# Optimization experiments

Hardware: AMD Instinct MI355X
Metric: run time of the kernel (lower is better)

## Reference

```python
import jax, jax.numpy as jnp
import numpy as np

NUM_HEADS = 8
BN_EPS = 1e-5


def setup_inputs() -> dict:
    key = jax.random.key(0)
    ks = jax.random.split(key, 7)
    B, C, T, N = 16, 512, 128, 64
    x = jax.random.normal(ks[0], (B, C, T, N), dtype=jnp.float32)
    # 1x1 convs stored as [out, in] matrices
    w_qkv = jax.random.normal(ks[1], (3 * C, C), dtype=jnp.float32) * (1.0 / np.sqrt(C))
    b_qkv = jax.random.normal(ks[2], (3 * C,), dtype=jnp.float32) * 0.01
    w_proj = jax.random.normal(ks[3], (C, C), dtype=jnp.float32) * (1.0 / np.sqrt(C))
    b_proj = jax.random.normal(ks[4], (C,), dtype=jnp.float32) * 0.01
    gamma = jnp.ones((C,), dtype=jnp.float32) + 0.1 * jax.random.normal(ks[5], (C,), dtype=jnp.float32)
    beta = 0.1 * jax.random.normal(ks[6], (C,), dtype=jnp.float32)
    return {"x": x, "w_qkv": w_qkv, "b_qkv": b_qkv, "w_proj": w_proj,
            "b_proj": b_proj, "gamma": gamma, "beta": beta}


def reference(x, w_qkv, b_qkv, w_proj, b_proj, gamma, beta):
    B, C, T, N = x.shape
    H = NUM_HEADS
    hd = C // H
    scale = 1.0 / np.sqrt(hd).astype(np.float32)

    # qkv 1x1 conv: [B,3C,T,N]
    qkv = jnp.einsum('bctn,oc->botn', x, w_qkv) + b_qkv[None, :, None, None]
    q, k, v = jnp.split(qkv, 3, axis=1)

    def to_heads(t):  # [B,C,T,N] -> [B,H,T,N,hd]
        return t.reshape(B, H, hd, T, N).transpose(0, 1, 3, 4, 2)

    q, k, v = to_heads(q), to_heads(k), to_heads(v)

    # unnormalized attention over the N (node) axis, no softmax
    attn = jnp.einsum('bhtnd,bhtmd->bhtnm', q, k) * scale  # [B,H,T,N,N]
    out = jnp.einsum('bhtnm,bhtmd->bhtnd', attn, v)        # [B,H,T,N,hd]

    # back to [B,C,T,N]
    out = out.transpose(0, 1, 4, 2, 3).reshape(B, C, T, N)

    # proj 1x1 conv
    out = jnp.einsum('bctn,oc->botn', out, w_proj) + b_proj[None, :, None, None]

    # BatchNorm2d (training-mode batch statistics, biased variance, eps=1e-5)
    mean = out.mean(axis=(0, 2, 3))
    var = out.var(axis=(0, 2, 3))
    out = (out - mean[None, :, None, None]) * (gamma / jnp.sqrt(var + BN_EPS))[None, :, None, None] \
          + beta[None, :, None, None]

    return out + x
```

## Files before the change

kernel.cpp:

```cpp
#include <hip/hip_runtime.h>

typedef unsigned int uint;
typedef unsigned short ushort;
typedef short short8 __attribute__((ext_vector_type(8)));
typedef float floatx4 __attribute__((ext_vector_type(4)));
typedef ushort ushortx8 __attribute__((ext_vector_type(8)));
typedef ushort ushortx4 __attribute__((ext_vector_type(4)));
typedef uint uintx4 __attribute__((ext_vector_type(4)));

#define DEV static __device__ __forceinline__

#define Bsz 16
#define Cch 512
#define Tt 128
#define Nn 64
#define Hh 8
#define HD 64
#define Pp 8192
#define BPOS 131072
#define C3 1536

DEV int swz(int row, int c8) { return row * 8 + (c8 ^ (row & 7) ^ ((row >> 3) & 7)); }

DEV ushort f2bf(float f) {
  uint u = __float_as_uint(f);
  return (ushort)((u + 0x7FFFu + ((u >> 16) & 1u)) >> 16);
}
DEV float bf2f(ushort h) { return __uint_as_float(((uint)h) << 16); }

DEV void gll16(const ushort* src, ushort* dst) {
  __builtin_amdgcn_global_load_lds(
      (const __attribute__((address_space(1))) unsigned int*)src,
      (__attribute__((address_space(3))) unsigned int*)dst, 16, 0, 0);
}

__global__ __launch_bounds__(256) void k_cvt(const float* __restrict__ src,
                                             ushort* __restrict__ dst, int n) {
  int gid = blockIdx.x * 256 + threadIdx.x;
  int i8 = gid * 8;
  if (i8 < n) {
    floatx4 a = *(const floatx4*)&src[i8];
    floatx4 b = *(const floatx4*)&src[i8 + 4];
    ushortx8 o;
#pragma unroll
    for (int j = 0; j < 4; ++j) { o[j] = f2bf(a[j]); o[j + 4] = f2bf(b[j]); }
    *(ushortx8*)&dst[i8] = o;
  }
}

__global__ __launch_bounds__(256) void k_transpose_x(const float* __restrict__ x,
                                                     ushort* __restrict__ xT) {
  int p0 = blockIdx.x * 64, c0 = blockIdx.y * 64, b = blockIdx.z;
  __shared__ __align__(16) ushort sm[4096];
  int tid = threadIdx.x;
  const float* xb = x + (size_t)b * Cch * Pp;
  ushort* xTb = xT + (size_t)b * Pp * Cch;
#pragma unroll
  for (int it = 0; it < 4; ++it) {
    int cc = tid + it * 256;
    int r = cc >> 4, c4 = cc & 15;
    floatx4 v = *(const floatx4*)&xb[(size_t)(c0 + r) * Pp + p0 + c4 * 4];
    ushortx4 o;
#pragma unroll
    for (int j = 0; j < 4; ++j) o[j] = f2bf(v[j]);
    *(ushortx4*)&sm[swz(r, c4 >> 1) * 8 + (c4 & 1) * 4] = o;
  }
  __syncthreads();
#pragma unroll
  for (int it = 0; it < 2; ++it) {
    int cc = tid + it * 256;
    int pl = cc >> 3, c8 = cc & 7;
    ushortx8 o;
#pragma unroll
    for (int j = 0; j < 8; ++j) {
      int c = c8 * 8 + j;
      o[j] = sm[swz(c, pl >> 3) * 8 + (pl & 7)];
    }
    *(ushortx8*)&xTb[(size_t)(p0 + pl) * Cch + c0 + c8 * 8] = o;
  }
}

__global__ __launch_bounds__(256) void k_gemm_bt(const ushort* __restrict__ A,
                                                 const ushort* __restrict__ W,
                                                 const float* __restrict__ bias,
                                                 ushort* __restrict__ D,
                                                 int K, int ldD,
                                                 size_t sAb, size_t sDb) {
  __shared__ __align__(16) ushort sm[32768];
  int tid = threadIdx.x;
  int lane = tid & 63, w = tid >> 6;
  int wm = (w & 1) * 64, wn = (w >> 1) * 64;
  size_t m0 = (size_t)blockIdx.y * 128;
  size_t n0 = (size_t)blockIdx.x * 128;
  const ushort* Ab = A + (size_t)blockIdx.z * sAb;
  ushort* Db = D + (size_t)blockIdx.z * sDb;

  const ushort *aS[4], *wS[4];
#pragma unroll
  for (int it = 0; it < 4; ++it) {
    int i = it * 256 + tid;
    int r = i >> 3;
    int c8 = (i & 7) ^ (r & 7) ^ ((r >> 3) & 7);
    aS[it] = &Ab[(m0 + r) * (size_t)K + c8 * 8];
    wS[it] = &W[(n0 + r) * (size_t)K + c8 * 8];
  }
  int dof = w * 512;

  floatx4 zero4 = {0.f, 0.f, 0.f, 0.f};
  floatx4 acc[4][4];
#pragma unroll
  for (int i = 0; i < 4; ++i)
#pragma unroll
    for (int j = 0; j < 4; ++j) acc[i][j] = zero4;

  const int NT = K >> 6;
#pragma unroll
  for (int it = 0; it < 4; ++it) {
    gll16(aS[it], &sm[it * 2048 + dof]);
    gll16(wS[it], &sm[8192 + it * 2048 + dof]);
  }
  __syncthreads();

  int cur = 0;
  for (int t = 0; t < NT; ++t) {
    ushort* cA = sm + (cur << 14);
    ushort* cB = cA + 8192;
    if (t + 1 < NT) {
      ushort* nA = sm + ((cur ^ 1) << 14);
      ushort* nB = nA + 8192;
      int kb = (t + 1) << 6;
#pragma unroll
      for (int it = 0; it < 4; ++it) {
        gll16(aS[it] + kb, &nA[it * 2048 + dof]);
        gll16(wS[it] + kb, &nB[it * 2048 + dof]);
      }
    }
#pragma unroll
    for (int kk = 0; kk < 2; ++kk) {
      int g = kk * 4 + (lane >> 4);
      int rr = lane & 15;
      short8 af[4], bf[4];
#pragma unroll
      for (int i = 0; i < 4; ++i) af[i] = *(const short8*)&cA[swz(wm + i * 16 + rr, g) * 8];
#pragma unroll
      for (int j = 0; j < 4; ++j) bf[j] = *(const short8*)&cB[swz(wn + j * 16 + rr, g) * 8];
#pragma unroll
      for (int i = 0; i < 4; ++i)
#pragma unroll
        for (int j = 0; j < 4; ++j)
          acc[i][j] = __builtin_amdgcn_mfma_f32_16x16x32_bf16(af[i], bf[j], acc[i][j], 0, 0, 0);
    }
    __syncthreads();
    cur ^= 1;
  }

  int quad = lane >> 4, col = lane & 15;
#pragma unroll
  for (int j = 0; j < 4; ++j) {
    int n_loc = wn + j * 16 + col;
    float bj = bias[n0 + n_loc];
#pragma unroll
    for (int i = 0; i < 4; ++i)
#pragma unroll
      for (int r = 0; r < 4; ++r) {
        int m_loc = wm + i * 16 + quad * 4 + r;
        sm[(m_loc * 16 + ((n_loc >> 3) ^ (m_loc & 7) ^ ((m_loc >> 3) & 7))) * 8 + (n_loc & 7)] =
            f2bf(acc[i][j][r] + bj);
      }
  }
  __syncthreads();
#pragma unroll
  for (int it = 0; it < 8; ++it) {
    int cc = tid + it * 256;
    int m_loc = cc >> 4, cn = cc & 15;
    uintx4 v = *(const uintx4*)&sm[(m_loc * 16 + (cn ^ (m_loc & 7) ^ ((m_loc >> 3) & 7))) * 8];
    *(uintx4*)&Db[(m0 + m_loc) * (size_t)ldD + n0 + cn * 8] = v;
  }
}

__global__ __launch_bounds__(256) void k_gemm2_t(const ushort* __restrict__ A,
                                                 const ushort* __restrict__ W,
                                                 const float* __restrict__ bias,
                                                 ushort* __restrict__ yL,
                                                 ushort* __restrict__ y0,
                                                 int K, int ldD,
                                                 size_t sAb, size_t sDb,
                                                 float* __restrict__ psum,
                                                 float* __restrict__ psq) {
  __shared__ __align__(16) ushort sm[32768];
  float* smf = (float*)sm;
  int tid = threadIdx.x;
  int lane = tid & 63, w = tid >> 6;
  int wm = (w & 1) * 64, wn = (w >> 1) * 64;
  size_t m0 = (size_t)blockIdx.y * 128;
  size_t n0 = (size_t)blockIdx.x * 128;
  const ushort* Ab = A + (size_t)blockIdx.z * sAb;
  ushort* Db = (blockIdx.z == 0) ? y0 : yL + (size_t)blockIdx.z * sDb;
  int part = blockIdx.z * 64 + blockIdx.y;

  const ushort *aS[4], *wS[4];
#pragma unroll
  for (int it = 0; it < 4; ++it) {
    int i = it * 256 + tid;
    int r = i >> 3;
    int c8 = (i & 7) ^ (r & 7) ^ ((r >> 3) & 7);
    aS[it] = &Ab[(m0 + r) * (size_t)K + c8 * 8];
    wS[it] = &W[(n0 + r) * (size_t)K + c8 * 8];
  }
  int dof = w * 512;

  floatx4 zero4 = {0.f, 0.f, 0.f, 0.f};
  floatx4 acc[4][4];
#pragma unroll
  for (int i = 0; i < 4; ++i)
#pragma unroll
    for (int j = 0; j < 4; ++j) acc[i][j] = zero4;

  const int NT = K >> 6;
#pragma unroll
  for (int it = 0; it < 4; ++it) {
    gll16(aS[it], &sm[it * 2048 + dof]);
    gll16(wS[it], &sm[8192 + it * 2048 + dof]);
  }
  __syncthreads();

  int cur = 0;
  for (int t = 0; t < NT; ++t) {
    ushort* cA = sm + (cur << 14);
    ushort* cB = cA + 8192;
    if (t + 1 < NT) {
      ushort* nA = sm + ((cur ^ 1) << 14);
      ushort* nB = nA + 8192;
      int kb = (t + 1) << 6;
#pragma unroll
      for (int it = 0; it < 4; ++it) {
        gll16(aS[it] + kb, &nA[it * 2048 + dof]);
        gll16(wS[it] + kb, &nB[it * 2048 + dof]);
      }
    }
#pragma unroll
    for (int kk = 0; kk < 2; ++kk) {
      int g = kk * 4 + (lane >> 4);
      int rr = lane & 15;
      short8 af[4], bf[4];
#pragma unroll
      for (int i = 0; i < 4; ++i) af[i] = *(const short8*)&cA[swz(wm + i * 16 + rr, g) * 8];
#pragma unroll
      for (int j = 0; j < 4; ++j) bf[j] = *(const short8*)&cB[swz(wn + j * 16 + rr, g) * 8];
#pragma unroll
      for (int i = 0; i < 4; ++i)
#pragma unroll
        for (int j = 0; j < 4; ++j)
          acc[i][j] = __builtin_amdgcn_mfma_f32_16x16x32_bf16(af[i], bf[j], acc[i][j], 0, 0, 0);
    }
    __syncthreads();
    cur ^= 1;
  }

  int quad = lane >> 4, col = lane & 15;
#pragma unroll
  for (int h = 0; h < 2; ++h) {
    __syncthreads();
    if ((w >> 1) == h) {
#pragma unroll
      for (int j = 0; j < 4; ++j) {
        int n1 = j * 16 + col;
        float bj = bias[n0 + h * 64 + n1];
#pragma unroll
        for (int i = 0; i < 4; ++i) {
          int mb = wm + i * 16 + quad * 4;
          floatx4 v4;
#pragma unroll
          for (int r = 0; r < 4; ++r) v4[r] = acc[i][j][r] + bj;
          *(floatx4*)&smf[n1 * 128 + (mb ^ ((n1 & 7) << 2))] = v4;
        }
      }
    }
    __syncthreads();
#pragma unroll
    for (int it = 0; it < 8; ++it) {
      int cc = tid + it * 256;
      int n2 = cc >> 5, ck = cc & 31;
      floatx4 v = *(const floatx4*)&smf[n2 * 128 + ((ck * 4) ^ ((n2 & 7) << 2))];
      ushortx4 o;
#pragma unroll
      for (int r = 0; r < 4; ++r) o[r] = f2bf(v[r]);
      *(ushortx4*)&Db[(n0 + h * 64 + n2) * (size_t)ldD + m0 + ck * 4] = o;
      float s = 0.f, q = 0.f;
#pragma unroll
      for (int r = 0; r < 4; ++r) {
        float f = bf2f(o[r]);
        s += f;
        q += f * f;
      }
#pragma unroll
      for (int off = 16; off > 0; off >>= 1) {
        s += __shfl_down(s, off, 32);
        q += __shfl_down(q, off, 32);
      }
      if ((tid & 31) == 0) {
        size_t c = n0 + h * 64 + n2;
        psum[c * 1024 + part] = s;
        psq[c * 1024 + part] = q;
      }
    }
  }
}

__global__ __launch_bounds__(256) void k_attn(const ushort* __restrict__ qkv,
                                              ushort* __restrict__ aT,
                                              size_t sQb, size_t sAb) {
  int bx = blockIdx.x;
  int t = bx & 127, h = bx >> 7;
  __shared__ __align__(16) ushort sm[16384];
  ushort* qs = sm;
  ushort* ks = sm + 4096;
  ushort* vt = sm + 8192;
  ushort* ss = sm + 12288;
  int tid = threadIdx.x, lane = tid & 63, w = tid >> 6;
  int quad = lane >> 4, col = lane & 15;
  const ushort* base = qkv + (size_t)blockIdx.y * sQb + (size_t)(t * 64) * C3 + h * 64;

#pragma unroll
  for (int it = 0; it < 2; ++it) {
    int i = it * 256 + tid;
    int r = i >> 3;
    int c8 = (i & 7) ^ (r & 7) ^ ((r >> 3) & 7);
    gll16(&base[(size_t)r * C3 + c8 * 8], &qs[(size_t)(it * 256 + w * 64) * 8]);
    gll16(&base[(size_t)r * C3 + 512 + c8 * 8], &ks[(size_t)(it * 256 + w * 64) * 8]);
    int n = i >> 3, d8 = i & 7;
    ushortx8 vv = *(const ushortx8*)&base[(size_t)n * C3 + 1024 + d8 * 8];
#pragma unroll
    for (int j = 0; j < 8; ++j) {
      int dp = d8 * 8 + j;
      vt[swz(dp, n >> 3) * 8 + (n & 7)] = vv[j];
    }
  }
  __syncthreads();

  floatx4 zero4 = {0.f, 0.f, 0.f, 0.f};
  floatx4 accs[4] = {zero4, zero4, zero4, zero4};
#pragma unroll
  for (int kk = 0; kk < 2; ++kk) {
    int g = kk * 4 + quad;
    short8 aq = *(const short8*)&qs[swz(w * 16 + col, g) * 8];
#pragma unroll
    for (int j = 0; j < 4; ++j) {
      short8 bk = *(const short8*)&ks[swz(j * 16 + col, g) * 8];
      accs[j] = __builtin_amdgcn_mfma_f32_16x16x32_bf16(aq, bk, accs[j], 0, 0, 0);
    }
  }
#pragma unroll
  for (int j = 0; j < 4; ++j)
#pragma unroll
    for (int r = 0; r < 4; ++r) {
      int n = w * 16 + quad * 4 + r, m = j * 16 + col;
      ss[swz(n, m >> 3) * 8 + (m & 7)] = f2bf(accs[j][r] * 0.125f);
    }
  __syncthreads();

  floatx4 acco[4] = {zero4, zero4, zero4, zero4};
#pragma unroll
  for (int kk = 0; kk < 2; ++kk) {
    int g = kk * 4 + quad;
    short8 as = *(const short8*)&ss[swz(w * 16 + col, g) * 8];
#pragma unroll
    for (int j = 0; j < 4; ++j) {
      short8 bv = *(const short8*)&vt[swz(j * 16 + col, g) * 8];
      acco[j] = __builtin_amdgcn_mfma_f32_16x16x32_bf16(as, bv, acco[j], 0, 0, 0);
    }
  }
#pragma unroll
  for (int j = 0; j < 4; ++j)
#pragma unroll
    for (int r = 0; r < 4; ++r) {
      int n = w * 16 + quad * 4 + r, dp = j * 16 + col;
      qs[swz(n, dp >> 3) * 8 + (dp & 7)] = f2bf(acco[j][r]);
    }
  __syncthreads();
  ushort* aTb = aT + (size_t)blockIdx.y * sAb + (size_t)(t * 64) * Cch + h * 64;
#pragma unroll
  for (int it = 0; it < 2; ++it) {
    int cc = tid + it * 256;
    int n = cc >> 3, c8 = cc & 7;
    uintx4 v = *(const uintx4*)&qs[swz(n, c8) * 8];
    *(uintx4*)&aTb[(size_t)n * Cch + c8 * 8] = v;
  }
}

__global__ __launch_bounds__(256) void k_bnfin(const float* __restrict__ psum,
                                               const float* __restrict__ psq,
                                               const float* __restrict__ gamma,
                                               const float* __restrict__ beta,
                                               float* __restrict__ scaleS,
                                               float* __restrict__ shiftS) {
  int c = blockIdx.x;
  int tid = threadIdx.x;
  floatx4 v = *(const floatx4*)&psum[(size_t)c * 1024 + tid * 4];
  floatx4 u = *(const floatx4*)&psq[(size_t)c * 1024 + tid * 4];
  float s = v[0] + v[1] + v[2] + v[3];
  float q = u[0] + u[1] + u[2] + u[3];
#pragma unroll
  for (int off = 32; off > 0; off >>= 1) {
    s += __shfl_down(s, off);
    q += __shfl_down(q, off);
  }
  __shared__ float rs[4], rq[4];
  if ((tid & 63) == 0) { rs[tid >> 6] = s; rq[tid >> 6] = q; }
  __syncthreads();
  if (tid == 0) {
    float S = rs[0] + rs[1] + rs[2] + rs[3];
    float Q = rq[0] + rq[1] + rq[2] + rq[3];
    float inv = 1.0f / (float)BPOS;
    float mean = S * inv;
    float var = Q * inv - mean * mean;
    float sc = gamma[c] * rsqrtf(var + 1e-5f);
    scaleS[c] = sc;
    shiftS[c] = beta[c] - mean * sc;
  }
}

__global__ __launch_bounds__(256) void k_final(const float* __restrict__ x,
                                               const ushort* __restrict__ y,
                                               float* __restrict__ out,
                                               const float* __restrict__ scaleS,
                                               const float* __restrict__ shiftS) {
  size_t gid = (size_t)blockIdx.x * 256 + threadIdx.x;
  size_t i8 = gid * 8;
  int c = (int)((i8 >> 13) & 511);
  float sc = scaleS[c], sh = shiftS[c];
  ushortx8 yv = *(const ushortx8*)&y[i8];
  floatx4 x0 = *(const floatx4*)&x[i8];
  floatx4 x1 = *(const floatx4*)&x[i8 + 4];
  floatx4 o0, o1;
#pragma unroll
  for (int j = 0; j < 4; ++j) {
    o0[j] = bf2f(yv[j]) * sc + sh + x0[j];
    o1[j] = bf2f(yv[j + 4]) * sc + sh + x1[j];
  }
  *(floatx4*)&out[i8] = o0;
  *(floatx4*)&out[i8 + 4] = o1;
}

extern "C" void kernel_launch(void* const* d_in, const int* in_sizes, int n_in,
                              void* d_out, int out_size, void* d_ws, size_t ws_size,
                              hipStream_t stream) {
  const float* x      = (const float*)d_in[0];
  const float* w_qkv  = (const float*)d_in[1];
  const float* b_qkv  = (const float*)d_in[2];
  const float* w_proj = (const float*)d_in[3];
  const float* b_proj = (const float*)d_in[4];
  const float* gamma  = (const float*)d_in[5];
  const float* beta   = (const float*)d_in[6];
  float* outf = (float*)d_out;

  char* ws = (char*)d_ws;
  float*  psum   = (float*)ws;
  float*  psq    = (float*)(ws + 2097152ull);
  ushort* y0ws   = (ushort*)(ws + 4194304ull);
  ushort* wqkvb  = (ushort*)(ws + 33554432ull);
  ushort* wprojb = (ushort*)(ws + 35127296ull);
  float*  st     = (float*)(ws + 35651584ull);
  float* scaleS = st, *shiftS = st + 512;

  ushort* xT   = (ushort*)((char*)d_out + 134217728ull);
  ushort* qkvL = (ushort*)d_out;
  ushort* yL   = (ushort*)d_out;

  const size_t PC = (size_t)Pp * Cch;
  const size_t PQ = (size_t)Pp * C3;
  const size_t CP = (size_t)Cch * Pp;

  k_cvt<<<dim3(384), 256, 0, stream>>>(w_qkv, wqkvb, 3 * Cch * Cch);
  k_cvt<<<dim3(128), 256, 0, stream>>>(w_proj, wprojb, Cch * Cch);
  k_transpose_x<<<dim3(Pp / 64, Cch / 64, Bsz), 256, 0, stream>>>(x, xT);

  for (int g = 0; g < 3; ++g) {
    int b0 = g * 5;
    k_gemm_bt<<<dim3(C3 / 128, Pp / 128, 5), 256, 0, stream>>>(
        xT + (size_t)b0 * PC, wqkvb, b_qkv, qkvL, Cch, C3, PC, PQ);
    k_attn<<<dim3(Hh * Tt, 5), 256, 0, stream>>>(qkvL, xT + (size_t)b0 * PC, PQ, PC);
  }
  k_gemm_bt<<<dim3(C3 / 128, Pp / 128, 1), 256, 0, stream>>>(
      xT + 15 * PC, wqkvb, b_qkv, qkvL, Cch, C3, 0, 0);
  k_attn<<<dim3(Hh * Tt, 1), 256, 0, stream>>>(qkvL, xT + 15 * PC, 0, 0);

  k_gemm2_t<<<dim3(Cch / 128, Pp / 128, 16), 256, 0, stream>>>(
      xT, wprojb, b_proj, yL, y0ws, Cch, Pp, PC, PC, psum, psq);

  k_bnfin<<<dim3(Cch), 256, 0, stream>>>(psum, psq, gamma, beta, scaleS, shiftS);

  k_final<<<dim3(8 * 2048), 256, 0, stream>>>(x + 8 * CP, yL + 8 * PC, outf + 8 * CP, scaleS, shiftS);
  k_final<<<dim3(4 * 2048), 256, 0, stream>>>(x + 4 * CP, yL + 4 * PC, outf + 4 * CP, scaleS, shiftS);
  k_final<<<dim3(2 * 2048), 256, 0, stream>>>(x + 2 * CP, yL + 2 * PC, outf + 2 * CP, scaleS, shiftS);
  k_final<<<dim3(1 * 2048), 256, 0, stream>>>(x + 1 * CP, yL + 1 * PC, outf + 1 * CP, scaleS, shiftS);
  k_final<<<dim3(1 * 2048), 256, 0, stream>>>(x, y0ws, outf, scaleS, shiftS);
}
```

Baseline: 1.157 ms.

## Fuse QKV projection and per-node attention into one kernel per (batch, t)

Replaces the batched QKV GEMM plus separate attention kernels with one fused kernel. Each block loads a 64-position by 512-channel input tile into LDS, then loops over heads: it computes Q/K/V with MFMA, forms the scores, applies them to V, and writes the result back in place. This removes the large QKV intermediate round-trip through global memory and several launches. In exchange, weights are read straight from global/L2 by every block with no LDS staging, and the 112KB of dynamic LDS limits occupancy to one block per CU.

```diff
diff --git a/kernel.cpp b/kernel.cpp
--- a/kernel.cpp
+++ b/kernel.cpp
@@ -80,101 +80,181 @@
   }
 }
 
-__global__ __launch_bounds__(256) void k_gemm_bt(const ushort* __restrict__ A,
-                                                 const ushort* __restrict__ W,
-                                                 const float* __restrict__ bias,
-                                                 ushort* __restrict__ D,
-                                                 int K, int ldD,
-                                                 size_t sAb, size_t sDb) {
-  __shared__ __align__(16) ushort sm[32768];
-  int tid = threadIdx.x;
-  int lane = tid & 63, w = tid >> 6;
-  int wm = (w & 1) * 64, wn = (w >> 1) * 64;
-  size_t m0 = (size_t)blockIdx.y * 128;
-  size_t n0 = (size_t)blockIdx.x * 128;
-  const ushort* Ab = A + (size_t)blockIdx.z * sAb;
-  ushort* Db = D + (size_t)blockIdx.z * sDb;
-
-  const ushort *aS[4], *wS[4];
-#pragma unroll
-  for (int it = 0; it < 4; ++it) {
+__global__ __launch_bounds__(256) void k_qkv_attn(ushort* __restrict__ xaT,
+                                                  const ushort* __restrict__ Wk,
+                                                  const float* __restrict__ bq) {
+  extern __shared__ __align__(16) ushort sm[];
+  int tid = threadIdx.x, lane = tid & 63, w = tid >> 6;
+  int pair = w >> 1, wh = w & 1;
+  int quad = lane >> 4, col = lane & 15;
+  int rr = col;
+  int t = blockIdx.x, b = blockIdx.y;
+  ushort* xb = xaT + ((size_t)b * Pp + (size_t)t * 64) * Cch;
+
+#pragma unroll
+  for (int it = 0; it < 16; ++it) {
     int i = it * 256 + tid;
-    int r = i >> 3;
+    int kt = i >> 9, r = (i >> 3) & 63;
     int c8 = (i & 7) ^ (r & 7) ^ ((r >> 3) & 7);
-    aS[it] = &Ab[(m0 + r) * (size_t)K + c8 * 8];
-    wS[it] = &W[(n0 + r) * (size_t)K + c8 * 8];
-  }
-  int dof = w * 512;
-
+    gll16(&xb[(size_t)r * Cch + kt * 64 + c8 * 8], &sm[(it * 256 + w * 64) * 8]);
+  }
+  __syncthreads();
+
+  ushort* qs = sm + 32768 + pair * 12288;
+  ushort* ks = qs + 4096;
+  ushort* vt = qs + 8192;
   floatx4 zero4 = {0.f, 0.f, 0.f, 0.f};
-  floatx4 acc[4][4];
-#pragma unroll
-  for (int i = 0; i < 4; ++i)
-#pragma unroll
-    for (int j = 0; j < 4; ++j) acc[i][j] = zero4;
-
-  const int NT = K >> 6;
-#pragma unroll
-  for (int it = 0; it < 4; ++it) {
-    gll16(aS[it], &sm[it * 2048 + dof]);
-    gll16(wS[it], &sm[8192 + it * 2048 + dof]);
-  }
-  __syncthreads();
-
-  int cur = 0;
-  for (int t = 0; t < NT; ++t) {
-    ushort* cA = sm + (cur << 14);
-    ushort* cB = cA + 8192;
-    if (t + 1 < NT) {
-      ushort* nA = sm + ((cur ^ 1) << 14);
-      ushort* nB = nA + 8192;
-      int kb = (t + 1) << 6;
-#pragma unroll
-      for (int it = 0; it < 4; ++it) {
-        gll16(aS[it] + kb, &nA[it * 2048 + dof]);
-        gll16(wS[it] + kb, &nB[it * 2048 + dof]);
-      }
-    }
+
+  for (int hh = 0; hh < 4; ++hh) {
+    int h = pair * 4 + hh;
+    int rowQK = wh * 512 + h * 64;
+    int rowV = 1024 + h * 64 + wh * 32;
+
+    floatx4 acc[4][4];
+#pragma unroll
+    for (int i2 = 0; i2 < 4; ++i2)
+#pragma unroll
+      for (int j = 0; j < 4; ++j) acc[i2][j] = zero4;
+#pragma unroll
+    for (int kt = 0; kt < 8; ++kt)
+#pragma unroll
+      for (int kk = 0; kk < 2; ++kk) {
+        int g = kk * 4 + (lane >> 4);
+        const ushort* wb = &Wk[(size_t)(rowQK + rr) * Cch + kt * 64 + g * 8];
+        short8 af[4], bf[4];
+#pragma unroll
+        for (int i2 = 0; i2 < 4; ++i2)
+          af[i2] = *(const short8*)&sm[kt * 4096 + swz(i2 * 16 + rr, g) * 8];
+#pragma unroll
+        for (int j = 0; j < 4; ++j) bf[j] = *(const short8*)&wb[(size_t)(j * 16) * Cch];
+#pragma unroll
+        for (int i2 = 0; i2 < 4; ++i2)
+#pragma unroll
+          for (int j = 0; j < 4; ++j)
+            acc[i2][j] = __builtin_amdgcn_mfma_f32_16x16x32_bf16(af[i2], bf[j], acc[i2][j], 0, 0, 0);
+      }
+    {
+      ushort* dqk = wh ? ks : qs;
+#pragma unroll
+      for (int j = 0; j < 4; ++j) {
+        int d = j * 16 + col;
+        float bj = bq[rowQK + d];
+#pragma unroll
+        for (int i2 = 0; i2 < 4; ++i2)
+#pragma unroll
+          for (int r = 0; r < 4; ++r) {
+            int n = i2 * 16 + quad * 4 + r;
+            dqk[swz(n, d >> 3) * 8 + (d & 7)] = f2bf(acc[i2][j][r] + bj);
+          }
+      }
+    }
+
+    floatx4 accv[4][2];
+#pragma unroll
+    for (int i2 = 0; i2 < 4; ++i2)
+#pragma unroll
+      for (int j = 0; j < 2; ++j) accv[i2][j] = zero4;
+#pragma unroll
+    for (int kt = 0; kt < 8; ++kt)
+#pragma unroll
+      for (int kk = 0; kk < 2; ++kk) {
+        int g = kk * 4 + (lane >> 4);
+        const ushort* wb = &Wk[(size_t)(rowV + rr) * Cch + kt * 64 + g * 8];
+        short8 af[4], bf[2];
+#pragma unroll
+        for (int i2 = 0; i2 < 4; ++i2)
+          af[i2] = *(const short8*)&sm[kt * 4096 + swz(i2 * 16 + rr, g) * 8];
+#pragma unroll
+        for (int j = 0; j < 2; ++j) bf[j] = *(const short8*)&wb[(size_t)(j * 16) * Cch];
+#pragma unroll
+        for (int i2 = 0; i2 < 4; ++i2)
+#pragma unroll
+          for (int j = 0; j < 2; ++j)
+            accv[i2][j] = __builtin_amdgcn_mfma_f32_16x16x32_bf16(af[i2], bf[j], accv[i2][j], 0, 0, 0);
+      }
+#pragma unroll
+    for (int j = 0; j < 2; ++j) {
+      int d = wh * 32 + j * 16 + col;
+      float bj = bq[1024 + h * 64 + d];
+#pragma unroll
+      for (int i2 = 0; i2 < 4; ++i2)
+#pragma unroll
+        for (int r = 0; r < 4; ++r) {
+          int n = i2 * 16 + quad * 4 + r;
+          vt[swz(d, n >> 3) * 8 + (n & 7)] = f2bf(accv[i2][j][r] + bj);
+        }
+    }
+    __syncthreads();
+
+    floatx4 accs[4][2];
+#pragma unroll
+    for (int i2 = 0; i2 < 4; ++i2)
+#pragma unroll
+      for (int j = 0; j < 2; ++j) accs[i2][j] = zero4;
 #pragma unroll
     for (int kk = 0; kk < 2; ++kk) {
       int g = kk * 4 + (lane >> 4);
-      int rr = lane & 15;
-      short8 af[4], bf[4];
-#pragma unroll
-      for (int i = 0; i < 4; ++i) af[i] = *(const short8*)&cA[swz(wm + i * 16 + rr, g) * 8];
-#pragma unroll
-      for (int j = 0; j < 4; ++j) bf[j] = *(const short8*)&cB[swz(wn + j * 16 + rr, g) * 8];
-#pragma unroll
-      for (int i = 0; i < 4; ++i)
-#pragma unroll
-        for (int j = 0; j < 4; ++j)
-          acc[i][j] = __builtin_amdgcn_mfma_f32_16x16x32_bf16(af[i], bf[j], acc[i][j], 0, 0, 0);
-    }
-    __syncthreads();
-    cur ^= 1;
-  }
-
-  int quad = lane >> 4, col = lane & 15;
-#pragma unroll
-  for (int j = 0; j < 4; ++j) {
-    int n_loc = wn + j * 16 + col;
-    float bj = bias[n0 + n_loc];
-#pragma unroll
-    for (int i = 0; i < 4; ++i)
-#pragma unroll
-      for (int r = 0; r < 4; ++r) {
-        int m_loc = wm + i * 16 + quad * 4 + r;
-        sm[(m_loc * 16 + ((n_loc >> 3) ^ (m_loc & 7) ^ ((m_loc >> 3) & 7))) * 8 + (n_loc & 7)] =
-            f2bf(acc[i][j][r] + bj);
-      }
-  }
-  __syncthreads();
-#pragma unroll
-  for (int it = 0; it < 8; ++it) {
-    int cc = tid + it * 256;
-    int m_loc = cc >> 4, cn = cc & 15;
-    uintx4 v = *(const uintx4*)&sm[(m_loc * 16 + (cn ^ (m_loc & 7) ^ ((m_loc >> 3) & 7))) * 8];
-    *(uintx4*)&Db[(m0 + m_loc) * (size_t)ldD + n0 + cn * 8] = v;
+      short8 aq[4], bk[2];
+#pragma unroll
+      for (int i2 = 0; i2 < 4; ++i2) aq[i2] = *(const short8*)&qs[swz(i2 * 16 + rr, g) * 8];
+#pragma unroll
+      for (int j = 0; j < 2; ++j) bk[j] = *(const short8*)&ks[swz(wh * 32 + j * 16 + rr, g) * 8];
+#pragma unroll
+      for (int i2 = 0; i2 < 4; ++i2)
+#pragma unroll
+        for (int j = 0; j < 2; ++j)
+          accs[i2][j] = __builtin_amdgcn_mfma_f32_16x16x32_bf16(aq[i2], bk[j], accs[i2][j], 0, 0, 0);
+    }
+    __syncthreads();
+#pragma unroll
+    for (int j = 0; j < 2; ++j)
+#pragma unroll
+      for (int i2 = 0; i2 < 4; ++i2)
+#pragma unroll
+        for (int r = 0; r < 4; ++r) {
+          int n = i2 * 16 + quad * 4 + r, m = wh * 32 + j * 16 + col;
+          qs[swz(n, m >> 3) * 8 + (m & 7)] = f2bf(accs[i2][j][r] * 0.125f);
+        }
+    __syncthreads();
+
+    floatx4 acco[4][2];
+#pragma unroll
+    for (int i2 = 0; i2 < 4; ++i2)
+#pragma unroll
+      for (int j = 0; j < 2; ++j) acco[i2][j] = zero4;
+#pragma unroll
+    for (int kk = 0; kk < 2; ++kk) {
+      int g = kk * 4 + (lane >> 4);
+      short8 as[4], bv[2];
+#pragma unroll
+      for (int i2 = 0; i2 < 4; ++i2) as[i2] = *(const short8*)&qs[swz(i2 * 16 + rr, g) * 8];
+#pragma unroll
+      for (int j = 0; j < 2; ++j) bv[j] = *(const short8*)&vt[swz(wh * 32 + j * 16 + rr, g) * 8];
+#pragma unroll
+      for (int i2 = 0; i2 < 4; ++i2)
+#pragma unroll
+        for (int j = 0; j < 2; ++j)
+          acco[i2][j] = __builtin_amdgcn_mfma_f32_16x16x32_bf16(as[i2], bv[j], acco[i2][j], 0, 0, 0);
+    }
+#pragma unroll
+    for (int j = 0; j < 2; ++j)
+#pragma unroll
+      for (int i2 = 0; i2 < 4; ++i2)
+#pragma unroll
+        for (int r = 0; r < 4; ++r) {
+          int n = i2 * 16 + quad * 4 + r, d = wh * 32 + j * 16 + col;
+          ks[swz(n, d >> 3) * 8 + (d & 7)] = f2bf(acco[i2][j][r]);
+        }
+    __syncthreads();
+
+#pragma unroll
+    for (int it = 0; it < 4; ++it) {
+      int cc = it * 128 + wh * 64 + lane;
+      int n = cc >> 3, c8 = cc & 7;
+      uintx4 v = *(const uintx4*)&ks[swz(n, c8) * 8];
+      *(uintx4*)&xb[(size_t)n * Cch + h * 64 + c8 * 8] = v;
+    }
+    __syncthreads();
   }
 }
 
@@ -307,87 +387,6 @@
   }
 }
 
-__global__ __launch_bounds__(256) void k_attn(const ushort* __restrict__ qkv,
-                                              ushort* __restrict__ aT,
-                                              size_t sQb, size_t sAb) {
-  int bx = blockIdx.x;
-  int t = bx & 127, h = bx >> 7;
-  __shared__ __align__(16) ushort sm[16384];
-  ushort* qs = sm;
-  ushort* ks = sm + 4096;
-  ushort* vt = sm + 8192;
-  ushort* ss = sm + 12288;
-  int tid = threadIdx.x, lane = tid & 63, w = tid >> 6;
-  int quad = lane >> 4, col = lane & 15;
-  const ushort* base = qkv + (size_t)blockIdx.y * sQb + (size_t)(t * 64) * C3 + h * 64;
-
-#pragma unroll
-  for (int it = 0; it < 2; ++it) {
-    int i = it * 256 + tid;
-    int r = i >> 3;
-    int c8 = (i & 7) ^ (r & 7) ^ ((r >> 3) & 7);
-    gll16(&base[(size_t)r * C3 + c8 * 8], &qs[(size_t)(it * 256 + w * 64) * 8]);
-    gll16(&base[(size_t)r * C3 + 512 + c8 * 8], &ks[(size_t)(it * 256 + w * 64) * 8]);
-    int n = i >> 3, d8 = i & 7;
-    ushortx8 vv = *(const ushortx8*)&base[(size_t)n * C3 + 1024 + d8 * 8];
-#pragma unroll
-    for (int j = 0; j < 8; ++j) {
-      int dp = d8 * 8 + j;
-      vt[swz(dp, n >> 3) * 8 + (n & 7)] = vv[j];
-    }
-  }
-  __syncthreads();
-
-  floatx4 zero4 = {0.f, 0.f, 0.f, 0.f};
-  floatx4 accs[4] = {zero4, zero4, zero4, zero4};
-#pragma unroll
-  for (int kk = 0; kk < 2; ++kk) {
-    int g = kk * 4 + quad;
-    short8 aq = *(const short8*)&qs[swz(w * 16 + col, g) * 8];
-#pragma unroll
-    for (int j = 0; j < 4; ++j) {
-      short8 bk = *(const short8*)&ks[swz(j * 16 + col, g) * 8];
-      accs[j] = __builtin_amdgcn_mfma_f32_16x16x32_bf16(aq, bk, accs[j], 0, 0, 0);
-    }
-  }
-#pragma unroll
-  for (int j = 0; j < 4; ++j)
-#pragma unroll
-    for (int r = 0; r < 4; ++r) {
-      int n = w * 16 + quad * 4 + r, m = j * 16 + col;
-      ss[swz(n, m >> 3) * 8 + (m & 7)] = f2bf(accs[j][r] * 0.125f);
-    }
-  __syncthreads();
-
-  floatx4 acco[4] = {zero4, zero4, zero4, zero4};
-#pragma unroll
-  for (int kk = 0; kk < 2; ++kk) {
-    int g = kk * 4 + quad;
-    short8 as = *(const short8*)&ss[swz(w * 16 + col, g) * 8];
-#pragma unroll
-    for (int j = 0; j < 4; ++j) {
-      short8 bv = *(const short8*)&vt[swz(j * 16 + col, g) * 8];
-      acco[j] = __builtin_amdgcn_mfma_f32_16x16x32_bf16(as, bv, acco[j], 0, 0, 0);
-    }
-  }
-#pragma unroll
-  for (int j = 0; j < 4; ++j)
-#pragma unroll
-    for (int r = 0; r < 4; ++r) {
-      int n = w * 16 + quad * 4 + r, dp = j * 16 + col;
-      qs[swz(n, dp >> 3) * 8 + (dp & 7)] = f2bf(acco[j][r]);
-    }
-  __syncthreads();
-  ushort* aTb = aT + (size_t)blockIdx.y * sAb + (size_t)(t * 64) * Cch + h * 64;
-#pragma unroll
-  for (int it = 0; it < 2; ++it) {
-    int cc = tid + it * 256;
-    int n = cc >> 3, c8 = cc & 7;
-    uintx4 v = *(const uintx4*)&qs[swz(n, c8) * 8];
-    *(uintx4*)&aTb[(size_t)n * Cch + c8 * 8] = v;
-  }
-}
-
 __global__ __launch_bounds__(256) void k_bnfin(const float* __restrict__ psum,
                                                const float* __restrict__ psq,
                                                const float* __restrict__ gamma,
@@ -463,27 +462,24 @@
   float*  st     = (float*)(ws + 35651584ull);
   float* scaleS = st, *shiftS = st + 512;
 
-  ushort* xT   = (ushort*)((char*)d_out + 134217728ull);
-  ushort* qkvL = (ushort*)d_out;
-  ushort* yL   = (ushort*)d_out;
+  ushort* xT = (ushort*)((char*)d_out + 134217728ull);
+  ushort* yL = (ushort*)d_out;
 
   const size_t PC = (size_t)Pp * Cch;
-  const size_t PQ = (size_t)Pp * C3;
   const size_t CP = (size_t)Cch * Pp;
+
+  static bool attrSet = false;
+  if (!attrSet) {
+    (void)hipFuncSetAttribute((const void*)k_qkv_attn,
+                              hipFuncAttributeMaxDynamicSharedMemorySize, 114688);
+    attrSet = true;
+  }
 
   k_cvt<<<dim3(384), 256, 0, stream>>>(w_qkv, wqkvb, 3 * Cch * Cch);
   k_cvt<<<dim3(128), 256, 0, stream>>>(w_proj, wprojb, Cch * Cch);
   k_transpose_x<<<dim3(Pp / 64, Cch / 64, Bsz), 256, 0, stream>>>(x, xT);
 
-  for (int g = 0; g < 3; ++g) {
-    int b0 = g * 5;
-    k_gemm_bt<<<dim3(C3 / 128, Pp / 128, 5), 256, 0, stream>>>(
-        xT + (size_t)b0 * PC, wqkvb, b_qkv, qkvL, Cch, C3, PC, PQ);
-    k_attn<<<dim3(Hh * Tt, 5), 256, 0, stream>>>(qkvL, xT + (size_t)b0 * PC, PQ, PC);
-  }
-  k_gemm_bt<<<dim3(C3 / 128, Pp / 128, 1), 256, 0, stream>>>(
-      xT + 15 * PC, wqkvb, b_qkv, qkvL, Cch, C3, 0, 0);
-  k_attn<<<dim3(Hh * Tt, 1), 256, 0, stream>>>(qkvL, xT + 15 * PC, 0, 0);
+  k_qkv_attn<<<dim3(Tt, Bsz), 256, 114688, stream>>>(xT, wqkvb, b_qkv);
 
   k_gemm2_t<<<dim3(Cch / 128, Pp / 128, 16), 256, 0, stream>>>(
       xT, wprojb, b_proj, yL, y0ws, Cch, Pp, PC, PC, psum, psq);
```

Result: slower. 1.250 ms (+8.0%).
